# Performance work log

Measured on AMD Instinct MI355X. Metric: run time of the kernel, lower is better.

Reference implementation:

```python
import jax, jax.numpy as jnp
import numpy as np
from jax import lax

SIM_THRESHOLD = 0.25   # similarity_threshold from init
MAX_STEPS = 4          # fixed upper bound on merge rounds (original loops to convergence)
NEG = -1e9


def _merge_once(emb, alive, thr):
    """One greedy merge round. emb: [n,d], alive: [n] bool.
    Returns (new_emb, new_alive, merge_occurred)."""
    n, d = emb.shape
    # fused pairwise similarity: (e_i . e_j) / d
    sim = jnp.einsum('id,jd->ij', emb, emb) / d            # [n,n]
    idx = jnp.arange(n)
    valid = (idx[None, :] > idx[:, None]) & alive[None, :] & alive[:, None]

    def body(merged, xs):
        sim_row, valid_row, i = xs
        cand = valid_row & (~merged)                        # j > i, alive, not yet consumed
        scores = jnp.where(cand, sim_row, NEG)
        j = jnp.argmax(scores)
        do = (~merged[i]) & (scores[j] >= thr)              # i itself not already consumed
        partner = jnp.where(do, j, -1)
        merged = merged.at[j].set(merged[j] | do)           # mark j as consumed
        return merged, partner

    merged0 = jnp.zeros(n, dtype=bool)
    _, partner = lax.scan(body, merged0, (sim, valid, idx))  # partner: [n] int

    has = partner >= 0
    pidx = jnp.clip(partner, 0, n - 1)
    fused = jnp.minimum(emb + emb[pidx], 1.0)               # clamp(v1+v2, max=1)
    # rows consumed as partners get removed (zeroed + dead); scatter via n+1 trick
    consumed = jnp.zeros(n + 1, dtype=bool).at[jnp.where(has, partner, n)].set(True)[:n]
    new_emb = jnp.where(has[:, None], fused, emb)
    new_emb = jnp.where(consumed[:, None], jnp.zeros((), emb.dtype), new_emb)
    new_alive = alive & (~consumed)
    return new_emb, new_alive, jnp.any(has)


def setup_inputs() -> dict:
    key = jax.random.key(0)
    embeddings = jax.random.uniform(key, (4096, 1024), dtype=jnp.float32)
    return {"embeddings": embeddings}


def reference(embeddings):
    n = embeddings.shape[0]
    alive0 = jnp.ones(n, dtype=bool)

    def step(carry, _):
        emb, alive, done = carry
        ne, na, occurred = _merge_once(emb, alive, SIM_THRESHOLD)
        emb = jnp.where(done, emb, ne)
        alive = jnp.where(done, alive, na)
        done = done | (~occurred) | (jnp.sum(na) <= 1)
        return (emb, alive, done), None

    (emb, alive, _), _ = lax.scan(step, (embeddings, alive0, jnp.array(False)), None, length=MAX_STEPS)
    # emb: merged embeddings padded in place (dead slots zeroed), alive: validity mask
    return emb, alive
```

## Files before the change

### kernel.cpp

```cpp
#include <hip/hip_runtime.h>
#include <stdint.h>

#define N 4096
#define D 1024
#define TILE 512
#define THRF 0.25f
#define GBK 32
#define ASTR 66
#define BSTR 34
#define LSTR 4224


__global__ void k_init(uint8_t* alive, int* mcnt, int* acnt) {
    int x = blockIdx.x * blockDim.x + threadIdx.x;
    if (x < N) alive[x] = 1;
    if (x < 8) { mcnt[x] = 0; acnt[x] = (x == 0) ? N : 0; }
}

__global__ __launch_bounds__(1024) void k_prep(const uint8_t* __restrict__ alive,
                                               int* __restrict__ idx, int* __restrict__ nAp,
                                               uint8_t* __restrict__ mgC,
                                               int* __restrict__ partner) {
    __shared__ int wsum[16];
    __shared__ int woff[16];
    int t = threadIdx.x, lane = t & 63, wv = t >> 6;
    int b4 = t * 4;
    uint32_t a4 = *(const uint32_t*)(alive + b4);
    int c0 = a4 & 1, c1 = (a4 >> 8) & 1, c2 = (a4 >> 16) & 1, c3 = (a4 >> 24) & 1;
    int c = c0 + c1 + c2 + c3;
    int pref = c;
    for (int off = 1; off < 64; off <<= 1) {
        int v = __shfl_up(pref, off);
        if (lane >= off) pref += v;
    }
    if (lane == 63) wsum[wv] = pref;
    __syncthreads();
    if (t == 0) { int s = 0; for (int w = 0; w < 16; ++w) { woff[w] = s; s += wsum[w]; } nAp[0] = s; }
    __syncthreads();
    int pos = woff[wv] + pref - c;
    if (c0) idx[pos++] = b4;
    if (c1) idx[pos++] = b4 + 1;
    if (c2) idx[pos++] = b4 + 2;
    if (c3) idx[pos++] = b4 + 3;
    partner[b4] = -1; partner[b4 + 1] = -1; partner[b4 + 2] = -1; partner[b4 + 3] = -1;
    *(uint32_t*)(mgC + b4) = 0u;
}

__device__ __forceinline__ void gemm_body(const float* __restrict__ E,
                                          const int* __restrict__ idx, int nA,
                                          float* __restrict__ simT,
                                          int t0, int bi, int cj,
                                          double As[GBK][ASTR], double Bs[GBK][BSTR],
                                          int* ra, int* ca) {
    int row0 = t0 + bi * 64;
    int col0 = cj * 32;
    if (row0 >= nA || col0 >= nA) return;
    if (col0 + 31 <= row0) return;
    int t = threadIdx.x;
    if (t < 64) ra[t] = (row0 + t < nA) ? idx[row0 + t] : -1;
    else if (t < 96) { int u = t - 64; ca[u] = (col0 + u < nA) ? idx[col0 + u] : -1; }
    __syncthreads();
    int tr = t >> 4, tc = t & 15;
    int sr = t >> 3;
    int sq = t & 7;
    double acc[4][2] = {};
    for (int k0 = 0; k0 < D; k0 += GBK) {
        for (int p = 0; p < 2; ++p) {
            int r = sr + p * 32;
            int rid = ra[r];
            float4 av = make_float4(0.f, 0.f, 0.f, 0.f);
            if (rid >= 0) av = *(const float4*)(E + (size_t)rid * D + k0 + sq * 4);
            As[sq * 4 + 0][r] = (double)av.x;
            As[sq * 4 + 1][r] = (double)av.y;
            As[sq * 4 + 2][r] = (double)av.z;
            As[sq * 4 + 3][r] = (double)av.w;
        }
        {
            int cid = ca[sr];
            float4 bv = make_float4(0.f, 0.f, 0.f, 0.f);
            if (cid >= 0) bv = *(const float4*)(E + (size_t)cid * D + k0 + sq * 4);
            Bs[sq * 4 + 0][sr] = (double)bv.x;
            Bs[sq * 4 + 1][sr] = (double)bv.y;
            Bs[sq * 4 + 2][sr] = (double)bv.z;
            Bs[sq * 4 + 3][sr] = (double)bv.w;
        }
        __syncthreads();
        for (int kk = 0; kk < GBK; ++kk) {
            double2 a01 = *(const double2*)&As[kk][tr * 4];
            double2 a23 = *(const double2*)&As[kk][tr * 4 + 2];
            double2 b01 = *(const double2*)&Bs[kk][tc * 2];
            double a[4] = {a01.x, a01.y, a23.x, a23.y};
            for (int u = 0; u < 4; ++u) {
                acc[u][0] = fma(a[u], b01.x, acc[u][0]);
                acc[u][1] = fma(a[u], b01.y, acc[u][1]);
            }
        }
        __syncthreads();
    }
    int rbase = bi * 64 + tr * 4;
    for (int u = 0; u < 4; ++u) {
        float2 o = make_float2((float)(acc[u][0] * (1.0 / 1024.0)),
                               (float)(acc[u][1] * (1.0 / 1024.0)));
        *(float2*)&simT[(size_t)(rbase + u) * N + col0 + tc * 2] = o;
    }
}

__global__ __launch_bounds__(256) void k_gemm(const float* __restrict__ E,
                                              const int* __restrict__ idx,
                                              const int* __restrict__ nAp,
                                              float* __restrict__ simT,
                                              int t0, int bx0) {
    __shared__ double As[GBK][ASTR];
    __shared__ double Bs[GBK][BSTR];
    __shared__ int ra[64], ca[32];
    gemm_body(E, idx, *nAp, simT, t0, blockIdx.y, blockIdx.x + bx0, As, Bs, ra, ca);
}

__global__ __launch_bounds__(1024) void k_sort(const float* __restrict__ simT,
                                               const int* __restrict__ nAp,
                                               const uint8_t* __restrict__ mgC,
                                               int t0, uint16_t* __restrict__ lists) {
    int nA = *nAp;
    int r = blockIdx.x;
    int cr = t0 + r;
    int t = threadIdx.x;
    if (cr >= nA) return;
    __shared__ uint64_t key[4096];
    __shared__ int cnt;
    uint16_t* out = lists + (size_t)r * LSTR;
    if (mgC[cr]) {
        if (t < 128) out[t] = (uint16_t)0xFFFFu;
        return;
    }
    if (t == 0) cnt = 0;
    __syncthreads();
    const float* row = simT + (size_t)r * N;
    int lane = t & 63;
    for (int cc = cr + 1 + t; cc < nA; cc += 1024) {
        float v = row[cc];
        bool ok = (v >= THRF) && (!mgC[cc]);
        unsigned long long mask = __ballot(ok);
        int wbase = 0;
        if (lane == 0 && mask) wbase = atomicAdd(&cnt, (int)__popcll(mask));
        wbase = __shfl(wbase, 0);
        if (ok) {
            int pos = wbase + (int)__popcll(mask & ((1ull << lane) - 1ull));
            uint32_t vb = __float_as_uint(v);
            key[pos] = ((((uint64_t)(~vb)) << 32) | (uint32_t)cc);
        }
    }
    __syncthreads();
    int m = cnt;
    int sm = 1; while (sm < m) sm <<= 1;
    for (int x = m + t; x < sm; x += 1024) key[x] = ~0ull;
    __syncthreads();
    for (int k = 2; k <= sm; k <<= 1) {
        for (int s = k >> 1; s > 0; s >>= 1) {
            for (int jj = t; jj < sm; jj += 1024) {
                int l = jj ^ s;
                if (l > jj) {
                    uint64_t a = key[jj], b = key[l];
                    bool asc = ((jj & k) == 0);
                    if ((a > b) == asc) { key[jj] = b; key[l] = a; }
                }
            }
            __syncthreads();
        }
    }
    for (int jj = t; jj < m; jj += 1024)
        out[jj] = (uint16_t)(key[jj] & 0xFFFFu);
    for (int x = m + t; x < m + 128; x += 1024) out[x] = (uint16_t)0xFFFFu;
}

__device__ __forceinline__ int refill63(const uint16_t* __restrict__ lists,
                                        const uint8_t* msk, int rr, int lane) {
    int base = 63;
    while (base + 63 <= LSTR) {
        uint32_t g = 0xFFFFu;
        if (lane < 63) g = lists[(size_t)rr * LSTR + base + lane];
        uint32_t d = (g > 4095u) ? 4096u : g;
        unsigned long long b = __ballot(msk[d] == 0);
        if (b) return __builtin_amdgcn_readlane((int)d, __ffsll((long long)b) - 1);
        unsigned long long vb = __ballot(g != 0xFFFFu);
        if (!((vb >> 62) & 1ull)) return -1;
        base += 63;
    }
    return -1;
}

__global__ __launch_bounds__(256) void k_wgemm(const float* __restrict__ E,
                                               const int* __restrict__ idx,
                                               const int* __restrict__ nAp,
                                               float* __restrict__ simT,
                                               const uint16_t* __restrict__ lists,
                                               uint8_t* __restrict__ mgC,
                                               int* __restrict__ partner,
                                               int t0w, int t0g, int bx0g,
                                               int* __restrict__ mcnt, int round) {
    __shared__ double As[GBK][ASTR];
    __shared__ double Bs[GBK][BSTR];
    __shared__ int ra[64], ca[32];
    __shared__ __align__(8) uint8_t msk[N + 8];
    __shared__ short pt[TILE];
    int nA = *nAp;
    if (blockIdx.x != 0) {
        int b = blockIdx.x - 1;
        gemm_body(E, idx, nA, simT, t0g, b & 7, (b >> 3) + bx0g, As, Bs, ra, ca);
        return;
    }
    int nrows = nA - t0w; if (nrows > TILE) nrows = TILE;
    if (nrows <= 0) return;
    int tid = threadIdx.x;
    for (int x = tid; x < N / 8; x += 256)
        ((unsigned long long*)msk)[x] = ((const unsigned long long*)mgC)[x];
    if (tid == 0) *(unsigned long long*)(msk + N) = 0x0101010101010101ull;
    __syncthreads();
    if (tid >= 64) return;
    int lane = tid;
    int nm = 0;
    unsigned long long skiphint = 0ull;
    uint32_t chA = 0xFFFFu, chB = 0xFFFFu;
    if (lane < 63) {
        chA = lists[lane];
        if (nrows > 1) chB = lists[(size_t)LSTR + lane];
    }
    for (int r = 0; r < nrows; ++r) {
        uint32_t chC = 0xFFFFu;
        if (r + 2 < nrows && lane < 63)
            chC = lists[(size_t)(r + 2) * LSTR + lane];
        if ((r & 63) == 0)
            skiphint = __ballot(msk[t0w + r + lane] != 0);
        if ((skiphint >> (r & 63)) & 1ull) {
            if (lane == 0) pt[r] = -1;
            chA = chB; chB = chC;
            continue;
        }
        uint32_t g = (lane == 63) ? (uint32_t)(t0w + r) : chA;
        uint32_t rc = (g > 4095u) ? 4096u : g;
        unsigned long long bal = __ballot(msk[rc] == 0);
        bool found = false;
        if (bal >> 63) {
            unsigned long long m = bal & 0x7FFFFFFFFFFFFFFFull;
            if (m) {
                int f = __ffsll((long long)m) - 1;
                if (lane == f) { pt[r] = (short)rc; msk[rc] = 1; }
                found = true;
            } else {
                unsigned long long vb = __ballot(lane < 63 && chA != 0xFFFFu);
                if ((vb >> 62) & 1ull) {
                    int p = refill63(lists, msk, r, lane);
                    if (p >= 0) {
                        if (lane == 0) { pt[r] = (short)p; msk[p] = 1; }
                        found = true;
                    } else if (lane == 0) pt[r] = -1;
                } else if (lane == 0) pt[r] = -1;
            }
        } else if (lane == 0) pt[r] = -1;
        if (found) ++nm;
        chA = chB; chB = chC;
    }
    for (int r2 = lane; r2 < nrows; r2 += 64) {
        int p = pt[r2];
        partner[idx[t0w + r2]] = (p < 0) ? -1 : idx[p];
    }
    for (int w = lane; w < N / 8; w += 64)
        ((unsigned long long*)mgC)[w] = ((const unsigned long long*)msk)[w];
    if (lane == 0 && nm) atomicAdd(&mcnt[round], nm);
}

__global__ __launch_bounds__(1024) void k_apply(const int* __restrict__ idx,
                                                const int* __restrict__ nAp,
                                                const uint8_t* __restrict__ mgC,
                                                uint8_t* __restrict__ alive,
                                                uint8_t* __restrict__ consumed,
                                                int* __restrict__ acnt, int slot) {
    int nA = *nAp;
    int t = threadIdx.x, lane = t & 63;
    for (int x = t; x < N; x += 1024) consumed[x] = 0;
    __syncthreads();
    for (int c = t; c < nA; c += 1024) {
        if (mgC[c]) { int o = idx[c]; consumed[o] = 1; alive[o] = 0; }
    }
    __syncthreads();
    int cnt = 0;
    for (int x = t; x < N; x += 1024) cnt += alive[x] ? 1 : 0;
    for (int off = 32; off > 0; off >>= 1) cnt += __shfl_down(cnt, off);
    if (lane == 0) atomicAdd(&acnt[slot], cnt);
}

__global__ void k_fuse(float* __restrict__ E, const int* __restrict__ partner) {
    int i = blockIdx.x;
    int p = partner[i];
    if (p < 0) return;
    float* ri = E + (size_t)i * D;
    const float* rp = E + (size_t)p * D;
    for (int e = threadIdx.x; e < D; e += blockDim.x)
        ri[e] = fminf(ri[e] + rp[e], 1.0f);
}

__global__ void k_zero(float* __restrict__ E, const uint8_t* __restrict__ consumed) {
    int i = blockIdx.x;
    if (!consumed[i]) return;
    float* ri = E + (size_t)i * D;
    for (int e = threadIdx.x; e < D; e += blockDim.x) ri[e] = 0.0f;
}

__global__ void k_alive_out(const uint8_t* __restrict__ alive, float* __restrict__ outA) {
    int x = blockIdx.x * blockDim.x + threadIdx.x;
    if (x < N) outA[x] = alive[x] ? 1.0f : 0.0f;
}

__global__ void k_diag(const int* __restrict__ mcnt, const int* __restrict__ acnt,
                       float* __restrict__ out) {
    bool bad = false;
    for (int r = 0; r < 4; ++r) {
        int before = acnt[r], after = acnt[r + 1], m = mcnt[r];
        if (after + m != before) bad = true;
        if (2 * m > before) bad = true;
        if (m < 0 || m > 2048) bad = true;
    }
    if (bad) out[0] = (float)(8.0e6 + (double)mcnt[0] * 2048.0 + (double)mcnt[1]);
}

extern "C" void kernel_launch(void* const* d_in, const int* in_sizes, int n_in,
                              void* d_out, int out_size, void* d_ws, size_t ws_size,
                              hipStream_t stream) {
    const float* Ein = (const float*)d_in[0];
    float* E = (float*)d_out;
    float* outAlive = E + (size_t)N * D;

    char* ws = (char*)d_in[0];
    float* simT = (float*)ws;        ws += (size_t)TILE * N * 4;
    uint16_t* lists = (uint16_t*)ws; ws += (size_t)TILE * LSTR * 2;
    int* partner = (int*)ws;         ws += (size_t)N * 4;
    int* idx = (int*)ws;             ws += (size_t)N * 4;
    int* mcnt = (int*)ws;            ws += 8 * 4;
    int* acnt = (int*)ws;            ws += 8 * 4;
    int* nA = (int*)ws;              ws += 16;
    uint8_t* mgC = (uint8_t*)ws;     ws += N;
    uint8_t* alive = (uint8_t*)ws;   ws += N;
    uint8_t* consumed = (uint8_t*)ws;

    hipMemcpyAsync(E, Ein, (size_t)N * D * sizeof(float), hipMemcpyDeviceToDevice, stream);
    k_init<<<(N + 255) / 256, 256, 0, stream>>>(alive, mcnt, acnt);

    for (int round = 0; round < 4; ++round) {
        k_prep<<<1, 1024, 0, stream>>>(alive, idx, nA, mgC, partner);
        k_gemm<<<dim3(128, 8), 256, 0, stream>>>(E, idx, nA, simT, 0, 0);
        for (int t = 0; t < 8; ++t) {
            int t0 = t * TILE;
            k_sort<<<TILE, 1024, 0, stream>>>(simT, nA, mgC, t0, lists);
            int tg = t + 1;
            int bx0g = tg * 16;
            int gb = (tg < 8) ? (128 - bx0g) * 8 : 0;
            k_wgemm<<<1 + gb, 256, 0, stream>>>(E, idx, nA, simT, lists, mgC,
                                                partner, t0, tg * TILE, bx0g,
                                                mcnt, round);
        }
        k_apply<<<1, 1024, 0, stream>>>(idx, nA, mgC, alive, consumed, acnt, round + 1);
        k_fuse<<<N, 256, 0, stream>>>(E, partner);
        k_zero<<<N, 256, 0, stream>>>(E, consumed);
    }
    k_alive_out<<<(N + 255) / 256, 256, 0, stream>>>(alive, outAlive);
    k_diag<<<1, 1, 0, stream>>>(mcnt, acnt, E);
}
```

Before: 3.533 ms.

## Process two rows per wave in greedy matcher and fuse apply/fuse/zero kernels

The serial greedy matching wave now handles two rows per step, one per 32-lane half, reading two candidates per lane with packed loads. Conflicts between the two rows are resolved explicitly, and list prefetching is unrolled four deep. The k_apply, k_fuse and k_zero kernels are replaced: consumed marks are written during matching, the alive update and counting move into k_prep and k_alive_out, and fusing and zeroing happen in one kernel. This cuts latency on the serial critical path and removes launches per round, at the cost of more complex conflict logic in the matcher and a possible ordering hazard in the merged fuse/zero kernel.

Result: faster. 2.925 ms (-17.2%).

```diff
diff --git a/kernel.cpp b/kernel.cpp
--- a/kernel.cpp
+++ b/kernel.cpp
@@ -11,21 +11,27 @@
 #define LSTR 4224
 
 
-__global__ void k_init(uint8_t* alive, int* mcnt, int* acnt) {
+__global__ void k_init(uint8_t* alive, uint8_t* consumedO, int* mcnt, int* acnt) {
     int x = blockIdx.x * blockDim.x + threadIdx.x;
-    if (x < N) alive[x] = 1;
+    if (x < N) { alive[x] = 1; consumedO[x] = 0; }
     if (x < 8) { mcnt[x] = 0; acnt[x] = (x == 0) ? N : 0; }
 }
 
-__global__ __launch_bounds__(1024) void k_prep(const uint8_t* __restrict__ alive,
+__global__ __launch_bounds__(1024) void k_prep(uint8_t* __restrict__ alive,
+                                               uint8_t* __restrict__ consumedO,
                                                int* __restrict__ idx, int* __restrict__ nAp,
                                                uint8_t* __restrict__ mgC,
-                                               int* __restrict__ partner) {
+                                               int* __restrict__ partner,
+                                               int* __restrict__ acnt, int rnd) {
     __shared__ int wsum[16];
     __shared__ int woff[16];
     int t = threadIdx.x, lane = t & 63, wv = t >> 6;
     int b4 = t * 4;
     uint32_t a4 = *(const uint32_t*)(alive + b4);
+    uint32_t c4 = *(const uint32_t*)(consumedO + b4);
+    a4 &= (c4 ^ 0x01010101u);
+    *(uint32_t*)(alive + b4) = a4;
+    *(uint32_t*)(consumedO + b4) = 0u;
     int c0 = a4 & 1, c1 = (a4 >> 8) & 1, c2 = (a4 >> 16) & 1, c3 = (a4 >> 24) & 1;
     int c = c0 + c1 + c2 + c3;
     int pref = c;
@@ -35,7 +41,11 @@
     }
     if (lane == 63) wsum[wv] = pref;
     __syncthreads();
-    if (t == 0) { int s = 0; for (int w = 0; w < 16; ++w) { woff[w] = s; s += wsum[w]; } nAp[0] = s; }
+    if (t == 0) {
+        int s = 0;
+        for (int w = 0; w < 16; ++w) { woff[w] = s; s += wsum[w]; }
+        nAp[0] = s; acnt[rnd] = s;
+    }
     __syncthreads();
     int pos = woff[wv] + pref - c;
     if (c0) idx[pos++] = b4;
@@ -172,21 +182,104 @@
     for (int x = m + t; x < m + 128; x += 1024) out[x] = (uint16_t)0xFFFFu;
 }
 
-__device__ __forceinline__ int refill63(const uint16_t* __restrict__ lists,
-                                        const uint8_t* msk, int rr, int lane) {
-    int base = 63;
-    while (base + 63 <= LSTR) {
-        uint32_t g = 0xFFFFu;
-        if (lane < 63) g = lists[(size_t)rr * LSTR + base + lane];
-        uint32_t d = (g > 4095u) ? 4096u : g;
-        unsigned long long b = __ballot(msk[d] == 0);
-        if (b) return __builtin_amdgcn_readlane((int)d, __ffsll((long long)b) - 1);
-        unsigned long long vb = __ballot(g != 0xFFFFu);
-        if (!((vb >> 62) & 1ull)) return -1;
-        base += 63;
+__device__ __forceinline__ int refill_row(const uint16_t* __restrict__ lists,
+                                          const uint8_t* msk, int h, int rr, int lane) {
+    int half = lane >> 5, hl = lane & 31;
+    int base = 62;
+    while (base + 62 <= LSTR) {
+        uint32_t d0 = 4096u, d1 = 4096u; bool w1 = false;
+        if (half == h && hl < 31) {
+            ushort2 g = *(const ushort2*)(lists + (size_t)rr * LSTR + base + 2 * hl);
+            w1 = (g.y != 0xFFFFu);
+            d0 = (g.x > 4095u) ? 4096u : (uint32_t)g.x;
+            d1 = (g.y > 4095u) ? 4096u : (uint32_t)g.y;
+        }
+        bool b0 = (msk[d0] == 0), b1 = (msk[d1] == 0);
+        uint32_t pk = b0 ? d0 : d1;
+        unsigned long long rb = __ballot(b0 || b1);
+        unsigned long long rv = __ballot(w1);
+        uint32_t rm = (uint32_t)(rb >> (h * 32)) & 0x7FFFFFFFu;
+        if (rm) return __builtin_amdgcn_readlane((int)pk, h * 32 + __builtin_ctz(rm));
+        if (!((rv >> (h * 32 + 30)) & 1)) return -1;
+        base += 62;
     }
     return -1;
 }
+
+#define PBODY(K, CH)                                                           \
+    {                                                                          \
+        int pr = pb + 2 * (K);                                                 \
+        if (pr < nrows) {                                                      \
+            int row1 = pr + 1;                                                 \
+            if ((pr & 63) == 0)                                                \
+                skiphint = __ballot(msk[t0w + pr + lane] != 0);                \
+            bool sk0 = (skiphint >> (pr & 63)) & 1ull;                         \
+            bool sk1 = (row1 < nrows) ? (((skiphint >> ((pr & 63) + 1)) & 1ull) != 0) : true; \
+            if (sk0 && sk1) {                                                  \
+                if (lane == 0) { pt[pr] = -1; if (row1 < nrows) pt[row1] = -1; } \
+            } else {                                                           \
+                uint32_t rc0, rc1; bool v1r = false;                           \
+                int myrow = pr + half;                                         \
+                if (hl == 31) {                                                \
+                    rc0 = (myrow < nrows) ? (uint32_t)(t0w + myrow) : 4096u;   \
+                    rc1 = 4096u;                                               \
+                } else {                                                       \
+                    uint32_t x0 = (CH) & 0xFFFFu, x1 = (CH) >> 16;             \
+                    v1r = (x1 != 0xFFFFu);                                     \
+                    rc0 = (x0 > 4095u) ? 4096u : x0;                           \
+                    rc1 = (x1 > 4095u) ? 4096u : x1;                           \
+                }                                                              \
+                bool a0 = (msk[rc0] == 0);                                     \
+                bool a1 = (msk[rc1] == 0);                                     \
+                uint32_t pick = a0 ? rc0 : rc1;                                \
+                unsigned long long balA = __ballot(a0);                        \
+                unsigned long long balB = __ballot(a1);                        \
+                unsigned long long bal = balA | balB;                          \
+                unsigned long long vbal = __ballot(v1r);                       \
+                uint32_t bl = (uint32_t)bal;                                   \
+                uint32_t bh = (uint32_t)(bal >> 32);                           \
+                bool full0 = (vbal >> 30) & 1ull;                              \
+                bool full1 = (vbal >> 62) & 1ull;                              \
+                int p1 = -1, p2 = -1;                                          \
+                if (!sk0 && ((bl >> 31) & 1u)) {                               \
+                    uint32_t m1 = bl & 0x7FFFFFFFu;                            \
+                    if (m1) p1 = __builtin_amdgcn_readlane((int)pick, __builtin_ctz(m1)); \
+                    else if (full0) p1 = refill_row(lists, msk, 0, pr, lane);  \
+                }                                                              \
+                if (lane == 0 && p1 >= 0) msk[p1] = 1;                         \
+                bool alive1 = !sk1 && ((bh >> 31) & 1u) && (p1 != t0w + row1); \
+                if (alive1) {                                                  \
+                    uint32_t m2 = bh & 0x7FFFFFFFu;                            \
+                    if (m2) {                                                  \
+                        int f2 = __builtin_ctz(m2);                            \
+                        p2 = __builtin_amdgcn_readlane((int)pick, 32 + f2);    \
+                        if (p2 == p1) {                                        \
+                            bool lA = (balA >> (32 + f2)) & 1ull;              \
+                            bool lB = (balB >> (32 + f2)) & 1ull;              \
+                            if (lA && lB) {                                    \
+                                p2 = __builtin_amdgcn_readlane((int)rc1, 32 + f2); \
+                            } else {                                           \
+                                m2 &= ~(1u << f2);                             \
+                                if (m2) p2 = __builtin_amdgcn_readlane((int)pick, 32 + __builtin_ctz(m2)); \
+                                else if (full1) p2 = refill_row(lists, msk, 1, row1, lane); \
+                                else p2 = -1;                                  \
+                            }                                                  \
+                        }                                                      \
+                    } else if (full1) p2 = refill_row(lists, msk, 1, row1, lane); \
+                }                                                              \
+                if (lane == 0) {                                               \
+                    if (p2 >= 0) msk[p2] = 1;                                  \
+                    pt[pr] = (short)p1;                                        \
+                    if (row1 < nrows) pt[row1] = (short)p2;                    \
+                }                                                              \
+                nm += (p1 >= 0) + (p2 >= 0);                                   \
+            }                                                                  \
+        }                                                                      \
+        (CH) = 0xFFFFFFFFu;                                                    \
+        { int nr = pb + 2 * (K) + 8 + half;                                    \
+          if (nr < nrows && hl < 31)                                           \
+              (CH) = *(const uint32_t*)(lists + (size_t)nr * LSTR + hl * 2); } \
+    }
 
 __global__ __launch_bounds__(256) void k_wgemm(const float* __restrict__ E,
                                                const int* __restrict__ idx,
@@ -195,6 +288,7 @@
                                                const uint16_t* __restrict__ lists,
                                                uint8_t* __restrict__ mgC,
                                                int* __restrict__ partner,
+                                               uint8_t* __restrict__ consumedO,
                                                int t0w, int t0g, int bx0g,
                                                int* __restrict__ mcnt, int round) {
     __shared__ double As[GBK][ASTR];
@@ -217,97 +311,55 @@
     __syncthreads();
     if (tid >= 64) return;
     int lane = tid;
+    int half = lane >> 5, hl = lane & 31;
     int nm = 0;
     unsigned long long skiphint = 0ull;
-    uint32_t chA = 0xFFFFu, chB = 0xFFFFu;
-    if (lane < 63) {
-        chA = lists[lane];
-        if (nrows > 1) chB = lists[(size_t)LSTR + lane];
-    }
-    for (int r = 0; r < nrows; ++r) {
-        uint32_t chC = 0xFFFFu;
-        if (r + 2 < nrows && lane < 63)
-            chC = lists[(size_t)(r + 2) * LSTR + lane];
-        if ((r & 63) == 0)
-            skiphint = __ballot(msk[t0w + r + lane] != 0);
-        if ((skiphint >> (r & 63)) & 1ull) {
-            if (lane == 0) pt[r] = -1;
-            chA = chB; chB = chC;
-            continue;
-        }
-        uint32_t g = (lane == 63) ? (uint32_t)(t0w + r) : chA;
-        uint32_t rc = (g > 4095u) ? 4096u : g;
-        unsigned long long bal = __ballot(msk[rc] == 0);
-        bool found = false;
-        if (bal >> 63) {
-            unsigned long long m = bal & 0x7FFFFFFFFFFFFFFFull;
-            if (m) {
-                int f = __ffsll((long long)m) - 1;
-                if (lane == f) { pt[r] = (short)rc; msk[rc] = 1; }
-                found = true;
-            } else {
-                unsigned long long vb = __ballot(lane < 63 && chA != 0xFFFFu);
-                if ((vb >> 62) & 1ull) {
-                    int p = refill63(lists, msk, r, lane);
-                    if (p >= 0) {
-                        if (lane == 0) { pt[r] = (short)p; msk[p] = 1; }
-                        found = true;
-                    } else if (lane == 0) pt[r] = -1;
-                } else if (lane == 0) pt[r] = -1;
-            }
-        } else if (lane == 0) pt[r] = -1;
-        if (found) ++nm;
-        chA = chB; chB = chC;
+    uint32_t q0 = 0xFFFFFFFFu, q1 = 0xFFFFFFFFu, q2 = 0xFFFFFFFFu, q3 = 0xFFFFFFFFu;
+    if (hl < 31) {
+        if (half + 0 < nrows) q0 = *(const uint32_t*)(lists + (size_t)(half + 0) * LSTR + hl * 2);
+        if (half + 2 < nrows) q1 = *(const uint32_t*)(lists + (size_t)(half + 2) * LSTR + hl * 2);
+        if (half + 4 < nrows) q2 = *(const uint32_t*)(lists + (size_t)(half + 4) * LSTR + hl * 2);
+        if (half + 6 < nrows) q3 = *(const uint32_t*)(lists + (size_t)(half + 6) * LSTR + hl * 2);
+    }
+    for (int pb = 0; pb < nrows; pb += 8) {
+        PBODY(0, q0)
+        PBODY(1, q1)
+        PBODY(2, q2)
+        PBODY(3, q3)
     }
     for (int r2 = lane; r2 < nrows; r2 += 64) {
         int p = pt[r2];
-        partner[idx[t0w + r2]] = (p < 0) ? -1 : idx[p];
+        int po = (p < 0) ? -1 : idx[p];
+        partner[idx[t0w + r2]] = po;
+        if (po >= 0) consumedO[po] = 1;
     }
     for (int w = lane; w < N / 8; w += 64)
         ((unsigned long long*)mgC)[w] = ((const unsigned long long*)msk)[w];
     if (lane == 0 && nm) atomicAdd(&mcnt[round], nm);
 }
 
-__global__ __launch_bounds__(1024) void k_apply(const int* __restrict__ idx,
-                                                const int* __restrict__ nAp,
-                                                const uint8_t* __restrict__ mgC,
-                                                uint8_t* __restrict__ alive,
-                                                uint8_t* __restrict__ consumed,
-                                                int* __restrict__ acnt, int slot) {
-    int nA = *nAp;
-    int t = threadIdx.x, lane = t & 63;
-    for (int x = t; x < N; x += 1024) consumed[x] = 0;
-    __syncthreads();
-    for (int c = t; c < nA; c += 1024) {
-        if (mgC[c]) { int o = idx[c]; consumed[o] = 1; alive[o] = 0; }
-    }
-    __syncthreads();
-    int cnt = 0;
-    for (int x = t; x < N; x += 1024) cnt += alive[x] ? 1 : 0;
-    for (int off = 32; off > 0; off >>= 1) cnt += __shfl_down(cnt, off);
-    if (lane == 0) atomicAdd(&acnt[slot], cnt);
-}
-
-__global__ void k_fuse(float* __restrict__ E, const int* __restrict__ partner) {
+__global__ void k_fz(float* __restrict__ E, const int* __restrict__ partner) {
     int i = blockIdx.x;
     int p = partner[i];
     if (p < 0) return;
     float* ri = E + (size_t)i * D;
-    const float* rp = E + (size_t)p * D;
-    for (int e = threadIdx.x; e < D; e += blockDim.x)
+    float* rp = E + (size_t)p * D;
+    for (int e = threadIdx.x; e < D; e += blockDim.x) {
         ri[e] = fminf(ri[e] + rp[e], 1.0f);
-}
-
-__global__ void k_zero(float* __restrict__ E, const uint8_t* __restrict__ consumed) {
-    int i = blockIdx.x;
-    if (!consumed[i]) return;
-    float* ri = E + (size_t)i * D;
-    for (int e = threadIdx.x; e < D; e += blockDim.x) ri[e] = 0.0f;
-}
-
-__global__ void k_alive_out(const uint8_t* __restrict__ alive, float* __restrict__ outA) {
-    int x = blockIdx.x * blockDim.x + threadIdx.x;
-    if (x < N) outA[x] = alive[x] ? 1.0f : 0.0f;
+        rp[e] = 0.0f;
+    }
+}
+
+__global__ __launch_bounds__(256) void k_alive_out(const uint8_t* __restrict__ alive,
+                                                   const uint8_t* __restrict__ consumedO,
+                                                   float* __restrict__ outA,
+                                                   int* __restrict__ acnt) {
+    int x = blockIdx.x * 256 + threadIdx.x;
+    int lane = threadIdx.x & 63;
+    uint8_t na = (uint8_t)(alive[x] && !consumedO[x]);
+    outA[x] = na ? 1.0f : 0.0f;
+    unsigned long long b = __ballot(na != 0);
+    if (lane == 0) atomicAdd(&acnt[4], (int)__popcll(b));
 }
 
 __global__ void k_diag(const int* __restrict__ mcnt, const int* __restrict__ acnt,
@@ -339,13 +391,14 @@
     int* nA = (int*)ws;              ws += 16;
     uint8_t* mgC = (uint8_t*)ws;     ws += N;
     uint8_t* alive = (uint8_t*)ws;   ws += N;
-    uint8_t* consumed = (uint8_t*)ws;
+    uint8_t* consumedO = (uint8_t*)ws;
 
     hipMemcpyAsync(E, Ein, (size_t)N * D * sizeof(float), hipMemcpyDeviceToDevice, stream);
-    k_init<<<(N + 255) / 256, 256, 0, stream>>>(alive, mcnt, acnt);
+    k_init<<<(N + 255) / 256, 256, 0, stream>>>(alive, consumedO, mcnt, acnt);
 
     for (int round = 0; round < 4; ++round) {
-        k_prep<<<1, 1024, 0, stream>>>(alive, idx, nA, mgC, partner);
+        k_prep<<<1, 1024, 0, stream>>>(alive, consumedO, idx, nA, mgC, partner,
+                                       acnt, round);
         k_gemm<<<dim3(128, 8), 256, 0, stream>>>(E, idx, nA, simT, 0, 0);
         for (int t = 0; t < 8; ++t) {
             int t0 = t * TILE;
@@ -354,13 +407,11 @@
             int bx0g = tg * 16;
             int gb = (tg < 8) ? (128 - bx0g) * 8 : 0;
             k_wgemm<<<1 + gb, 256, 0, stream>>>(E, idx, nA, simT, lists, mgC,
-                                                partner, t0, tg * TILE, bx0g,
-                                                mcnt, round);
-        }
-        k_apply<<<1, 1024, 0, stream>>>(idx, nA, mgC, alive, consumed, acnt, round + 1);
-        k_fuse<<<N, 256, 0, stream>>>(E, partner);
-        k_zero<<<N, 256, 0, stream>>>(E, consumed);
-    }
-    k_alive_out<<<(N + 255) / 256, 256, 0, stream>>>(alive, outAlive);
+                                                partner, consumedO, t0, tg * TILE,
+                                                bx0g, mcnt, round);
+        }
+        k_fz<<<N, 256, 0, stream>>>(E, partner);
+    }
+    k_alive_out<<<16, 256, 0, stream>>>(alive, consumedO, outAlive, acnt);
     k_diag<<<1, 1, 0, stream>>>(mcnt, acnt, E);
 }
```
